# Kernel tuning notes

Measured on AMD Instinct MI355X. Metric: run time of the kernel, lower is better.

The kernel has to match this reference:

```python
import jax, jax.numpy as jnp
import numpy as np

D_MODEL = 1024
NUM_HEADS = 16
D_HEAD = 64  # d_q = d_k = d_v
BATCH = 4
SEQ = 2048


def _trunc_normal(key, shape, std):
    # truncated normal in [-3*std, 3*std], matching nn.init.trunc_normal_
    return jax.random.truncated_normal(key, -3.0, 3.0, shape, dtype=jnp.float32) * std


def setup_inputs() -> dict:
    key = jax.random.key(0)
    k_x, k_q, k_k, k_v, k_o = jax.random.split(key, 5)
    hd = NUM_HEADS * D_HEAD
    s_in = np.sqrt(2.0 / (D_MODEL + hd))
    s_out = np.sqrt(2.0 / (hd + D_MODEL))
    return {
        "in_features": jax.random.normal(k_x, (BATCH, SEQ, D_MODEL), dtype=jnp.float32),
        "w_q": _trunc_normal(k_q, (hd, D_MODEL), s_in),
        "w_k": _trunc_normal(k_k, (hd, D_MODEL), s_in),
        "w_v": _trunc_normal(k_v, (hd, D_MODEL), s_in),
        "w_o": _trunc_normal(k_o, (D_MODEL, hd), s_out),
    }


def reference(in_features, w_q, w_k, w_v, w_o):
    B, S, D = in_features.shape
    H, Dh = NUM_HEADS, D_HEAD
    # QKV projections (weight stored as [out, in])
    q = jnp.einsum('od,bsd->bso', w_q, in_features).reshape(B, S, H, Dh).transpose(0, 2, 1, 3)
    k = jnp.einsum('od,bsd->bso', w_k, in_features).reshape(B, S, H, Dh).transpose(0, 2, 1, 3)
    v = jnp.einsum('od,bsd->bso', w_v, in_features).reshape(B, S, H, Dh).transpose(0, 2, 1, 3)
    # scaled dot-product attention with dense causal mask (as in source)
    att = jnp.einsum('bhqd,bhkd->bhqk', q, k) / jnp.sqrt(jnp.float32(Dh)).astype(q.dtype)
    causal = jnp.tril(jnp.ones((S, S), dtype=bool))
    att = jnp.where(causal, att, -jnp.inf)
    att = jax.nn.softmax(att, axis=-1)
    out = jnp.einsum('bhqk,bhkd->bhqd', att, v)  # [B,H,S,Dh]
    out = out.transpose(0, 2, 1, 3).reshape(B, S, H * Dh)
    return jnp.einsum('od,bsd->bso', w_o, out)
```

## Files before the change

### kernel.cpp

```cpp
#include <hip/hip_runtime.h>
#include <stdint.h>

#define D_MODEL 1024
#define NHEADS  16
#define DHEAD   64
#define BATCH   4
#define SEQ     2048
#define MTOT    (BATCH*SEQ)

typedef unsigned short u16;
typedef uint32_t u32;
typedef __bf16 bf16x8 __attribute__((ext_vector_type(8)));
typedef float  f32x4  __attribute__((ext_vector_type(4)));
typedef float  f32x16 __attribute__((ext_vector_type(16)));
typedef u16    u16x8  __attribute__((ext_vector_type(8)));
typedef u16    u16x4  __attribute__((ext_vector_type(4)));
typedef u32    u32x4  __attribute__((ext_vector_type(4)));

__device__ __forceinline__ u16 f2bf(float f) {
  uint32_t u = __builtin_bit_cast(uint32_t, f);
  u += 0x7fff + ((u >> 16) & 1);
  return (u16)(u >> 16);
}

__device__ __forceinline__ void gll16(const u16* g, u16* lds) {
  __builtin_amdgcn_global_load_lds(
      (__attribute__((address_space(1))) void*)(g),
      (__attribute__((address_space(3))) void*)(lds), 16, 0, 0);
}

__global__ void cvtk(const float4* __restrict__ in, u16x4* __restrict__ out, int n4) {
  const int i = blockIdx.x * blockDim.x + threadIdx.x;
  if (i < n4) {
    const float4 f = in[i];
    u16x4 h;
    h[0] = f2bf(f.x); h[1] = f2bf(f.y); h[2] = f2bf(f.z); h[3] = f2bf(f.w);
    out[i] = h;
  }
}

template<int MODE>
__launch_bounds__(256)
__global__ void gemm_bt_k(const u16* __restrict__ A,
                          const u16* __restrict__ W0,
                          const u16* __restrict__ W1,
                          const u16* __restrict__ W2,
                          void* __restrict__ Cout)
{
  constexpr int K = D_MODEL;
  const int tid = threadIdx.x;
  const int l = tid & 63, w = tid >> 6;
  const int m0 = blockIdx.x * 128;
  const int n0 = blockIdx.y * 128;
  const u16* Bm = W0;
  float scale = 1.0f;
  if (MODE == 1) {
    const int z = blockIdx.z;
    Bm = (z == 0) ? W0 : ((z == 1) ? W1 : W2);
    scale = (z == 0) ? 0.125f * 1.44269504088896f : 1.0f;
  }

  __shared__ __align__(16) u16 As[128*32];
  __shared__ __align__(16) u16 Bs[128*32];

  f32x4 acc[4][4];
  #pragma unroll
  for (int i = 0; i < 4; ++i)
    #pragma unroll
    for (int j = 0; j < 4; ++j)
      acc[i][j] = f32x4{0.f, 0.f, 0.f, 0.f};

  const int wr = w >> 1, wc = w & 1;
  const int srow = l >> 2;
  const int scol = (l & 3) * 8;

  for (int k0 = 0; k0 < K; k0 += 32) {
    __syncthreads();
    #pragma unroll
    for (int j = 0; j < 2; ++j) {
      const int seg = w * 2 + j;
      gll16(A  + (size_t)(m0 + seg*16 + srow) * K + k0 + scol, &As[seg*512]);
      gll16(Bm + (size_t)(n0 + seg*16 + srow) * K + k0 + scol, &Bs[seg*512]);
    }
    __syncthreads();
    bf16x8 af[4], bfr[4];
    #pragma unroll
    for (int m = 0; m < 4; ++m)
      af[m] = *(const bf16x8*)&As[(wr*64 + m*16 + (l & 15))*32 + (l >> 4)*8];
    #pragma unroll
    for (int n = 0; n < 4; ++n)
      bfr[n] = *(const bf16x8*)&Bs[(wc*64 + n*16 + (l & 15))*32 + (l >> 4)*8];
    #pragma unroll
    for (int m = 0; m < 4; ++m)
      #pragma unroll
      for (int n = 0; n < 4; ++n)
        acc[m][n] = __builtin_amdgcn_mfma_f32_16x16x32_bf16(af[m], bfr[n], acc[m][n], 0, 0, 0);
  }

  const int g = l >> 4, c15 = l & 15;
  #pragma unroll
  for (int m = 0; m < 4; ++m) {
    #pragma unroll
    for (int n = 0; n < 4; ++n) {
      #pragma unroll
      for (int j = 0; j < 4; ++j) {
        const int row = m0 + wr*64 + m*16 + g*4 + j;
        const int col = n0 + wc*64 + n*16 + c15;
        const float v = acc[m][n][j] * scale;
        if (MODE == 0) {
          ((float*)Cout)[(size_t)row * D_MODEL + col] = v;
        } else {
          const int b = row >> 11, s = row & (SEQ-1);
          const int h = col >> 6, dh = col & (DHEAD-1);
          ((u16*)Cout)[(size_t)blockIdx.z * MTOT * D_MODEL
                       + ((size_t)(b*NHEADS + h) * SEQ + s) * DHEAD + dh] = f2bf(v);
        }
      }
    }
  }
}

__launch_bounds__(512)
__global__ void attn3_k(const u16* __restrict__ Qb, const u16* __restrict__ Kb_,
                        const u16* __restrict__ Vb_, u16* __restrict__ Oa)
{
  const int tid = threadIdx.x;
  const int w = tid >> 6, l = tid & 63;
  const int q5 = l & 31, hi = l >> 5;
  const int r = blockIdx.x;
  const int bh = (r & 7) * 8 + ((r >> 3) & 7);
  const int pairi = r >> 6;
  const int b = bh >> 4, h = bh & 15;
  const size_t base = (size_t)bh * SEQ * DHEAD;
  const u16* Qg = Qb + base;
  const u16* Kg = Kb_ + base;
  const u16* Vg = Vb_ + base;

  __shared__ __align__(16) u16 smem[16384];

  const int kc = tid & 7, row = tid >> 3;
  const int kr8 = l >> 3;
  const int kkv = 8*w + kr8;
  const int kdc = (l & 7) ^ kr8 ^ w;

  int vidx[8];
  #pragma unroll
  for (int e = 0; e < 8; ++e)
    vidx[e] = (8*kc + e)*64 + (((row >> 3) ^ kc ^ e) & 7)*8 + (row & 7);

  for (int half = 0; half < 2; ++half) {
    const int tq = half ? (7 - pairi) : pairi;
    const int q0w = tq*256 + 32*w;
    const int ntk = (tq + 1) * 4;
    const int ntw = (q0w >> 6) + 1;

    bf16x8 qf[4];
    #pragma unroll
    for (int s = 0; s < 4; ++s)
      qf[s] = *(const bf16x8*)(Qg + (size_t)(q0w + q5)*DHEAD + 16*s + 8*hi);

    f32x16 c0 = {}, c1 = {};
    float mrun = -1e30f, lrun = 0.f;

    {
      gll16(Kg + (size_t)kkv*DHEAD + kdc*8, smem + w*512);
      const u16x8 vr0 = *(const u16x8*)(Vg + (size_t)row*DHEAD + kc*8);
      #pragma unroll
      for (int e = 0; e < 8; ++e) smem[8192 + vidx[e]] = vr0[e];
    }
    __syncthreads();

    for (int t = 0; t < ntk; ++t) {
      const int cur = t & 1;
      const bool pf = (t + 1 < ntk);
      u16x8 vr;
      if (pf) {
        vr = *(const u16x8*)(Vg + (size_t)((t+1)*64 + row)*DHEAD + kc*8);
        gll16(Kg + (size_t)((t+1)*64 + kkv)*DHEAD + kdc*8,
              smem + (cur^1)*4096 + w*512);
      }

      if (t < ntw) {
        const u16* Kb = smem + cur*4096;
        const u16* Vv = smem + 8192 + cur*4096;

        f32x16 st[2] = {{}, {}};
        __builtin_amdgcn_s_setprio(1);
        #pragma unroll
        for (int kb = 0; kb < 2; ++kb) {
          #pragma unroll
          for (int s = 0; s < 4; ++s) {
            const int slot = ((2*s + hi) ^ (l & 7) ^ (4*kb) ^ (q5 >> 3)) & 7;
            const bf16x8 kf = *(const bf16x8*)(Kb + (32*kb + q5)*64 + slot*8);
            st[kb] = __builtin_amdgcn_mfma_f32_32x32x16_bf16(kf, qf[s], st[kb], 0, 0, 0);
          }
        }
        __builtin_amdgcn_s_setprio(0);

        if (t == ntw - 1) {
          const int kv0 = t*64;
          #pragma unroll
          for (int kb = 0; kb < 2; ++kb)
            #pragma unroll
            for (int rr = 0; rr < 16; ++rr) {
              const int kvg = kv0 + 32*kb + (rr & 3) + 8*(rr >> 2) + 4*hi;
              if (kvg > q0w + q5) st[kb][rr] = -1e30f;
            }
        }

        float mx = -1e30f;
        #pragma unroll
        for (int kb = 0; kb < 2; ++kb)
          #pragma unroll
          for (int rr = 0; rr < 16; ++rr) mx = fmaxf(mx, st[kb][rr]);
        mx = fmaxf(mx, __shfl_xor(mx, 32));
        const float mnew = fmaxf(mrun, mx);
        const float alpha = __builtin_amdgcn_exp2f(mrun - mnew);
        mrun = mnew;
        float rs = 0.f;
        #pragma unroll
        for (int kb = 0; kb < 2; ++kb)
          #pragma unroll
          for (int rr = 0; rr < 16; ++rr) {
            const float p = __builtin_amdgcn_exp2f(st[kb][rr] - mnew);
            st[kb][rr] = p;
            rs += p;
          }
        rs += __shfl_xor(rs, 32);
        lrun = lrun * alpha + rs;
        #pragma unroll
        for (int rr = 0; rr < 16; ++rr) { c0[rr] *= alpha; c1[rr] *= alpha; }

        bf16x8 pb[4];
        #pragma unroll
        for (int kb = 0; kb < 2; ++kb) {
          u32 pw[8];
          #pragma unroll
          for (int i = 0; i < 8; ++i) {
            u32 t0;
            asm("v_cvt_pk_bf16_f32 %0, %1, %2"
                : "=v"(t0) : "v"(st[kb][2*i]), "v"(st[kb][2*i+1]));
            pw[i] = t0;
          }
          asm("v_permlane32_swap_b32 %0, %1" : "+v"(pw[0]), "+v"(pw[2]));
          asm("v_permlane32_swap_b32 %0, %1" : "+v"(pw[1]), "+v"(pw[3]));
          asm("v_permlane32_swap_b32 %0, %1" : "+v"(pw[4]), "+v"(pw[6]));
          asm("v_permlane32_swap_b32 %0, %1" : "+v"(pw[5]), "+v"(pw[7]));
          pb[2*kb]   = __builtin_bit_cast(bf16x8, u32x4{pw[0], pw[1], pw[2], pw[3]});
          pb[2*kb+1] = __builtin_bit_cast(bf16x8, u32x4{pw[4], pw[5], pw[6], pw[7]});
        }

        __builtin_amdgcn_s_setprio(1);
        #pragma unroll
        for (int s = 0; s < 4; ++s) {
          {
            const int slot = ((2*s + hi) ^ (l & 7) ^ (q5 >> 3)) & 7;
            const bf16x8 vf = *(const bf16x8*)(Vv + q5*64 + slot*8);
            c0 = __builtin_amdgcn_mfma_f32_32x32x16_bf16(vf, pb[s], c0, 0, 0, 0);
          }
          {
            const int slot = ((2*s + hi) ^ (l & 7) ^ 4 ^ (q5 >> 3)) & 7;
            const bf16x8 vf = *(const bf16x8*)(Vv + (32 + q5)*64 + slot*8);
            c1 = __builtin_amdgcn_mfma_f32_32x32x16_bf16(vf, pb[s], c1, 0, 0, 0);
          }
        }
        __builtin_amdgcn_s_setprio(0);
      }

      if (pf) {
        u16* Vd = smem + 8192 + (cur^1)*4096;
        #pragma unroll
        for (int e = 0; e < 8; ++e) Vd[vidx[e]] = vr[e];
      }
      __syncthreads();
    }

    const float linv = __builtin_amdgcn_rcpf(lrun);
    #pragma unroll
    for (int Ab = 0; Ab < 2; ++Ab)
      #pragma unroll
      for (int rr = 0; rr < 16; ++rr) {
        const int d = 32*Ab + (rr & 3) + 8*(rr >> 2) + 4*hi;
        smem[w*2048 + q5*64 + (((d >> 3) ^ (q5 & 7)) & 7)*8 + (d & 7)] =
            f2bf((Ab ? c1[rr] : c0[rr]) * linv);
      }
    __syncthreads();
    #pragma unroll
    for (int cc = 0; cc < 4; ++cc) {
      const int dchunk = 4*hi + cc;
      const u16x8 vv = *(const u16x8*)&smem[w*2048 + q5*64 + ((dchunk ^ (q5 & 7)) & 7)*8];
      *(u16x8*)(Oa + (size_t)(b*SEQ + q0w + q5)*D_MODEL + h*DHEAD + 32*hi + 8*cc) = vv;
    }
    __syncthreads();
  }
}

extern "C" void kernel_launch(void* const* d_in, const int* in_sizes, int n_in,
                              void* d_out, int out_size, void* d_ws, size_t ws_size,
                              hipStream_t stream) {
  const float* X  = (const float*)d_in[0];
  const float* Wq = (const float*)d_in[1];
  const float* Wk = (const float*)d_in[2];
  const float* Wv = (const float*)d_in[3];
  const float* Wo = (const float*)d_in[4];

  u16* xb  = (u16*)d_ws;
  u16* wqb = xb  + (size_t)MTOT*D_MODEL;
  u16* wkb = wqb + (size_t)D_MODEL*D_MODEL;
  u16* wvb = wkb + (size_t)D_MODEL*D_MODEL;
  u16* wob = wvb + (size_t)D_MODEL*D_MODEL;
  u16* qkv = wob + (size_t)D_MODEL*D_MODEL;
  u16* att = qkv + (size_t)3*MTOT*D_MODEL;

  const int nx4 = MTOT*D_MODEL/4;
  const int nw4 = D_MODEL*D_MODEL/4;
  cvtk<<<nx4/256, 256, 0, stream>>>((const float4*)X,  (u16x4*)xb,  nx4);
  cvtk<<<nw4/256, 256, 0, stream>>>((const float4*)Wq, (u16x4*)wqb, nw4);
  cvtk<<<nw4/256, 256, 0, stream>>>((const float4*)Wk, (u16x4*)wkb, nw4);
  cvtk<<<nw4/256, 256, 0, stream>>>((const float4*)Wv, (u16x4*)wvb, nw4);
  cvtk<<<nw4/256, 256, 0, stream>>>((const float4*)Wo, (u16x4*)wob, nw4);

  dim3 g1(MTOT/128, D_MODEL/128, 3);
  gemm_bt_k<1><<<g1, 256, 0, stream>>>(xb, wqb, wkb, wvb, (void*)qkv);

  attn3_k<<<256, 512, 0, stream>>>(qkv, qkv + (size_t)MTOT*D_MODEL,
                                   qkv + (size_t)2*MTOT*D_MODEL, att);

  dim3 g3(MTOT/128, D_MODEL/128, 1);
  gemm_bt_k<0><<<g3, 256, 0, stream>>>(att, wob, nullptr, nullptr, d_out);
}
```

Before: 173.1 us.

## Shrink attention blocks to 128 queries, add lazy softmax rescale, fuse weight casts

```diff
diff --git a/kernel.cpp b/kernel.cpp
--- a/kernel.cpp
+++ b/kernel.cpp
@@ -37,6 +37,19 @@
     h[0] = f2bf(f.x); h[1] = f2bf(f.y); h[2] = f2bf(f.z); h[3] = f2bf(f.w);
     out[i] = h;
   }
+}
+
+__global__ void cvtk4(const float4* __restrict__ a, const float4* __restrict__ b,
+                      const float4* __restrict__ c, const float4* __restrict__ d,
+                      u16x4* __restrict__ out, int n4) {
+  const int i = blockIdx.x * blockDim.x + threadIdx.x;
+  if (i >= n4) return;
+  const float4* src = (blockIdx.y == 0) ? a : (blockIdx.y == 1) ? b
+                    : (blockIdx.y == 2) ? c : d;
+  const float4 f = src[i];
+  u16x4 h;
+  h[0] = f2bf(f.x); h[1] = f2bf(f.y); h[2] = f2bf(f.z); h[3] = f2bf(f.w);
+  out[(size_t)blockIdx.y * n4 + i] = h;
 }
 
 template<int MODE>
@@ -120,8 +133,8 @@
   }
 }
 
-__launch_bounds__(512)
-__global__ void attn3_k(const u16* __restrict__ Qb, const u16* __restrict__ Kb_,
+__launch_bounds__(256)
+__global__ void attn4_k(const u16* __restrict__ Qb, const u16* __restrict__ Kb_,
                         const u16* __restrict__ Vb_, u16* __restrict__ Oa)
 {
   const int tid = threadIdx.x;
@@ -138,21 +151,20 @@
 
   __shared__ __align__(16) u16 smem[16384];
 
-  const int kc = tid & 7, row = tid >> 3;
-  const int kr8 = l >> 3;
-  const int kkv = 8*w + kr8;
-  const int kdc = (l & 7) ^ kr8 ^ w;
-
-  int vidx[8];
+  const int kc = tid & 7, rp = tid >> 3;
+  int vIdx32[8];
   #pragma unroll
-  for (int e = 0; e < 8; ++e)
-    vidx[e] = (8*kc + e)*64 + (((row >> 3) ^ kc ^ e) & 7)*8 + (row & 7);
+  for (int e = 0; e < 8; ++e) {
+    const int d = 8*kc + e;
+    vIdx32[e] = d*32 + ((((rp >> 2) ^ kc ^ e) & 7) << 2) + (rp & 3);
+  }
+  const int krow = l >> 3, ksl = l & 7;
 
   for (int half = 0; half < 2; ++half) {
-    const int tq = half ? (7 - pairi) : pairi;
-    const int q0w = tq*256 + 32*w;
-    const int ntk = (tq + 1) * 4;
-    const int ntw = (q0w >> 6) + 1;
+    const int tq = half ? (15 - pairi) : pairi;
+    const int q0w = tq*128 + 32*w;
+    const int ntk = 2*tq + 2;
+    const int ntw = 2*tq + (w >> 1) + 1;
 
     bf16x8 qf[4];
     #pragma unroll
@@ -163,21 +175,31 @@
     float mrun = -1e30f, lrun = 0.f;
 
     {
-      gll16(Kg + (size_t)kkv*DHEAD + kdc*8, smem + w*512);
-      const u16x8 vr0 = *(const u16x8*)(Vg + (size_t)row*DHEAD + kc*8);
-      #pragma unroll
-      for (int e = 0; e < 8; ++e) smem[8192 + vidx[e]] = vr0[e];
+      #pragma unroll
+      for (int j = 0; j < 2; ++j)
+        gll16(Kg + (size_t)(16*w + 8*j + krow)*DHEAD + (size_t)((ksl ^ krow ^ (2*w + j)) & 7)*8,
+              smem + (w*128 + j*64)*8);
+      const u16x8 v0 = *(const u16x8*)(Vg + (size_t)(2*rp)*DHEAD + kc*8);
+      const u16x8 v1 = *(const u16x8*)(Vg + (size_t)(2*rp + 1)*DHEAD + kc*8);
+      u32* Vd = (u32*)(smem + 8192);
+      #pragma unroll
+      for (int e = 0; e < 8; ++e)
+        Vd[vIdx32[e]] = (u32)v0[e] | ((u32)v1[e] << 16);
     }
     __syncthreads();
 
     for (int t = 0; t < ntk; ++t) {
       const int cur = t & 1;
       const bool pf = (t + 1 < ntk);
-      u16x8 vr;
+      u16x8 v0, v1;
       if (pf) {
-        vr = *(const u16x8*)(Vg + (size_t)((t+1)*64 + row)*DHEAD + kc*8);
-        gll16(Kg + (size_t)((t+1)*64 + kkv)*DHEAD + kdc*8,
-              smem + (cur^1)*4096 + w*512);
+        const int kv1 = (t + 1)*64;
+        v0 = *(const u16x8*)(Vg + (size_t)(kv1 + 2*rp)*DHEAD + kc*8);
+        v1 = *(const u16x8*)(Vg + (size_t)(kv1 + 2*rp + 1)*DHEAD + kc*8);
+        #pragma unroll
+        for (int j = 0; j < 2; ++j)
+          gll16(Kg + (size_t)(kv1 + 16*w + 8*j + krow)*DHEAD + (size_t)((ksl ^ krow ^ (2*w + j)) & 7)*8,
+                smem + ((cur^1)*512 + w*128 + j*64)*8);
       }
 
       if (t < ntw) {
@@ -214,22 +236,25 @@
           #pragma unroll
           for (int rr = 0; rr < 16; ++rr) mx = fmaxf(mx, st[kb][rr]);
         mx = fmaxf(mx, __shfl_xor(mx, 32));
-        const float mnew = fmaxf(mrun, mx);
-        const float alpha = __builtin_amdgcn_exp2f(mrun - mnew);
-        mrun = mnew;
+        float alpha = 1.0f;
+        if (!__all(mx <= mrun + 8.0f)) {
+          const float mnew = fmaxf(mrun, mx);
+          alpha = __builtin_amdgcn_exp2f(mrun - mnew);
+          mrun = mnew;
+          #pragma unroll
+          for (int rr = 0; rr < 16; ++rr) { c0[rr] *= alpha; c1[rr] *= alpha; }
+        }
         float rs = 0.f;
         #pragma unroll
         for (int kb = 0; kb < 2; ++kb)
           #pragma unroll
           for (int rr = 0; rr < 16; ++rr) {
-            const float p = __builtin_amdgcn_exp2f(st[kb][rr] - mnew);
+            const float p = __builtin_amdgcn_exp2f(st[kb][rr] - mrun);
             st[kb][rr] = p;
             rs += p;
           }
         rs += __shfl_xor(rs, 32);
         lrun = lrun * alpha + rs;
-        #pragma unroll
-        for (int rr = 0; rr < 16; ++rr) { c0[rr] *= alpha; c1[rr] *= alpha; }
 
         bf16x8 pb[4];
         #pragma unroll
@@ -268,9 +293,10 @@
       }
 
       if (pf) {
-        u16* Vd = smem + 8192 + (cur^1)*4096;
-        #pragma unroll
-        for (int e = 0; e < 8; ++e) Vd[vidx[e]] = vr[e];
+        u32* Vd = (u32*)(smem + 8192) + (cur^1)*2048;
+        #pragma unroll
+        for (int e = 0; e < 8; ++e)
+          Vd[vIdx32[e]] = (u32)v0[e] | ((u32)v1[e] << 16);
       }
       __syncthreads();
     }
@@ -314,16 +340,16 @@
 
   const int nx4 = MTOT*D_MODEL/4;
   const int nw4 = D_MODEL*D_MODEL/4;
-  cvtk<<<nx4/256, 256, 0, stream>>>((const float4*)X,  (u16x4*)xb,  nx4);
-  cvtk<<<nw4/256, 256, 0, stream>>>((const float4*)Wq, (u16x4*)wqb, nw4);
-  cvtk<<<nw4/256, 256, 0, stream>>>((const float4*)Wk, (u16x4*)wkb, nw4);
-  cvtk<<<nw4/256, 256, 0, stream>>>((const float4*)Wv, (u16x4*)wvb, nw4);
-  cvtk<<<nw4/256, 256, 0, stream>>>((const float4*)Wo, (u16x4*)wob, nw4);
+  cvtk<<<nx4/256, 256, 0, stream>>>((const float4*)X, (u16x4*)xb, nx4);
+  dim3 gc(nw4/256, 4, 1);
+  cvtk4<<<gc, 256, 0, stream>>>((const float4*)Wq, (const float4*)Wk,
+                                (const float4*)Wv, (const float4*)Wo,
+                                (u16x4*)wqb, nw4);
 
   dim3 g1(MTOT/128, D_MODEL/128, 3);
   gemm_bt_k<1><<<g1, 256, 0, stream>>>(xb, wqb, wkb, wvb, (void*)qkv);
 
-  attn3_k<<<256, 512, 0, stream>>>(qkv, qkv + (size_t)MTOT*D_MODEL,
+  attn4_k<<<512, 256, 0, stream>>>(qkv, qkv + (size_t)MTOT*D_MODEL,
                                    qkv + (size_t)2*MTOT*D_MODEL, att);
 
   dim3 g3(MTOT/128, D_MODEL/128, 1);
```

After: 201.0 us. +16.1%, slower.
